# Optimization experiments

Hardware: AMD Instinct MI355X
Metric: run time of the kernel (lower is better)

Reference implementation:

```python
import jax, jax.numpy as jnp
import numpy as np
from jax import lax

B, C, H, W = 32, 512, 14, 14
NA = 9
N = H * W * NA  # 1764 anchors per image
IOU_THR = 0.3
SCORE_THR = 0.5
TOPK = 50


def setup_inputs() -> dict:
    key = jax.random.key(0)
    ks = jax.random.split(key, 8)
    def w(k, shape):
        return jax.random.normal(k, shape, jnp.float32) * 0.01  # nn.init.normal_(std=0.01)
    inp = {"features": jax.random.normal(ks[0], (B, C, H, W), jnp.float32)}
    # bbox head: 512->256 (GN32) ->128 (GN16) ->128 (GN16) -> 4*NA (1x1)
    inp["b1w"] = w(ks[1], (256, 512, 3, 3)); inp["b1b"] = jnp.zeros(256)
    inp["bg1w"] = jnp.ones(256); inp["bg1b"] = jnp.zeros(256)
    inp["b2w"] = w(ks[2], (128, 256, 3, 3)); inp["b2b"] = jnp.zeros(128)
    inp["bg2w"] = jnp.ones(128); inp["bg2b"] = jnp.zeros(128)
    inp["b3w"] = w(ks[3], (128, 128, 3, 3)); inp["b3b"] = jnp.zeros(128)
    inp["bg3w"] = jnp.ones(128); inp["bg3b"] = jnp.zeros(128)
    inp["b4w"] = w(ks[4], (4 * NA, 128, 1, 1)); inp["b4b"] = jnp.zeros(4 * NA)
    # classification head: 512->256 (GN32) ->128 (GN16) -> NA (1x1)
    inp["c1w"] = w(ks[5], (256, 512, 3, 3)); inp["c1b"] = jnp.zeros(256)
    inp["cg1w"] = jnp.ones(256); inp["cg1b"] = jnp.zeros(256)
    inp["c2w"] = w(ks[6], (128, 256, 3, 3)); inp["c2b"] = jnp.zeros(128)
    inp["cg2w"] = jnp.ones(128); inp["cg2b"] = jnp.zeros(128)
    inp["c3w"] = w(ks[7], (NA, 128, 1, 1)); inp["c3b"] = jnp.zeros(NA)
    return inp


def conv(x, w, b):
    k = w.shape[-1]
    pad = ((k // 2, k // 2), (k // 2, k // 2))
    y = lax.conv_general_dilated(x, w, (1, 1), pad, dimension_numbers=("NCHW", "OIHW", "NCHW"))
    return y + b[None, :, None, None]


def group_norm(x, w, b, groups, eps=1e-5):
    Bn, Cn, Hn, Wn = x.shape
    xg = x.reshape(Bn, groups, Cn // groups, Hn, Wn)
    mu = xg.mean(axis=(2, 3, 4), keepdims=True)
    var = xg.var(axis=(2, 3, 4), keepdims=True)
    xg = (xg - mu) * lax.rsqrt(var + eps)
    return xg.reshape(Bn, Cn, Hn, Wn) * w[None, :, None, None] + b[None, :, None, None]


def gelu(x):
    return jax.nn.gelu(x, approximate=False)  # torch nn.GELU default (erf)


def nms_single(boxes, scores):
    # boxes [N,4], scores [N]; greedy NMS, fixed-shape padded output [TOPK,5]
    valid = scores > SCORE_THR
    boxes = jnp.clip(boxes, 0.0, 1.0)
    order = jnp.argsort(-jnp.where(valid, scores, -jnp.inf))  # desc, invalid last
    b = boxes[order]; s = scores[order]; v = valid[order]
    x1 = jnp.maximum(b[:, None, 0], b[None, :, 0])
    y1 = jnp.maximum(b[:, None, 1], b[None, :, 1])
    x2 = jnp.minimum(b[:, None, 2], b[None, :, 2])
    y2 = jnp.minimum(b[:, None, 3], b[None, :, 3])
    inter = jnp.clip(x2 - x1, 0.0) * jnp.clip(y2 - y1, 0.0)
    area = (b[:, 2] - b[:, 0]) * (b[:, 3] - b[:, 1])
    iou = inter / (area[:, None] + area[None, :] - inter)
    # torch keeps when iou < thr; NaN compares False -> suppressed. Replicate exactly:
    suppress = jnp.logical_not(iou < IOU_THR)  # [N,N] bool
    idxs = jnp.arange(N)
    def body(suppressed, xs):
        row, i, vi = xs
        keep_i = vi & jnp.logical_not(suppressed[i])
        return suppressed | (keep_i & row & (idxs > i)), keep_i
    _, keep = lax.scan(body, jnp.zeros(N, bool), (suppress, idxs, v))
    kept_scores = jnp.where(keep, s, -1.0)
    topv, topi = lax.top_k(kept_scores, TOPK)  # first <=50 kept in score order
    out_boxes = jnp.where(topv[:, None] > 0.0, b[topi], 0.0)
    return jnp.concatenate([out_boxes, topv[:, None]], axis=-1)  # [TOPK, 5]; score=-1 marks pad


def _forward(features, b1w, b1b, bg1w, bg1b, b2w, b2b, bg2w, bg2b, b3w, b3b, bg3w, bg3b, b4w, b4b, c1w, c1b, cg1w, cg1b, c2w, c2b, cg2w, cg2b, c3w, c3b):
    bs = features.shape[0]
    h = group_norm(gelu(conv(features, b1w, b1b)), bg1w, bg1b, 32)
    h = group_norm(gelu(conv(h, b2w, b2b)), bg2w, bg2b, 16)
    h = group_norm(gelu(conv(h, b3w, b3b)), bg3w, bg3b, 16)
    bbox = conv(h, b4w, b4b).transpose(0, 2, 3, 1).reshape(bs, -1, 4)  # [B,N,4]
    h = group_norm(gelu(conv(features, c1w, c1b)), cg1w, cg1b, 32)
    h = group_norm(gelu(conv(h, c2w, c2b)), cg2w, cg2b, 16)
    conf = jax.nn.sigmoid(conv(h, c3w, c3b).transpose(0, 2, 3, 1).reshape(bs, -1))  # [B,N]
    return jax.vmap(nms_single)(bbox, conf)  # [B,TOPK,5]


def reference(features, b1w, b1b, bg1w, bg1b, b2w, b2b, bg2w, bg2b, b3w, b3b, bg3w, bg3b, b4w, b4b, c1w, c1b, cg1w, cg1b, c2w, c2b, cg2w, cg2b, c3w, c3b):
    return _forward(features, b1w, b1b, bg1w, bg1b, b2w, b2b, bg2w, bg2b, b3w, b3b, bg3w, bg3b, b4w, b4b, c1w, c1b, cg1w, cg1b, c2w, c2b, cg2w, cg2b, c3w, c3b)
```

## Files before the change

### kernel.cpp

```cpp
#include <hip/hip_runtime.h>
#include <hip/hip_bf16.h>
#include <math.h>

#define CHUNK 16
#define NN 1764
#define SORTN 2048

typedef float v2f __attribute__((ext_vector_type(2)));

template<int Co, int Ci>
__device__ inline void seg_pack_pk(const float* __restrict__ src, float* __restrict__ dst, int i) {
  int co = i / (Ci * 9); int rem = i - co * (Ci * 9); int ci = rem / 9; int k = rem - ci * 9;
  int p = (co >> 5) * 16 + (co & 15);
  int h = (co & 31) >> 4;
  dst[((size_t)ci * (Co >> 1) + p) * 20 + 2 * k + h] = src[i];
}
template<int Co, int CiK>
__device__ inline void seg_tr(const float* __restrict__ src, float* __restrict__ dst, int i) {
  int co = i / CiK; int cik = i - co * CiK;
  dst[cik * Co + co] = src[i];
}

__global__ void wtrans_all(
  const float* __restrict__ b1w, const float* __restrict__ c1w,
  const float* __restrict__ b2w, const float* __restrict__ c2w,
  const float* __restrict__ b3w, const float* __restrict__ b4w,
  const float* __restrict__ c3w,
  float* __restrict__ wp1b, float* __restrict__ wp1c,
  float* __restrict__ wp2b, float* __restrict__ wp2c,
  float* __restrict__ wp3b, float* __restrict__ wt4b, float* __restrict__ wt3c)
{
  int j = blockIdx.x * blockDim.x + threadIdx.x;
  if (j < 1179648) { seg_pack_pk<256, 512>(b1w, wp1b, j); return; } j -= 1179648;
  if (j < 1179648) { seg_pack_pk<256, 512>(c1w, wp1c, j); return; } j -= 1179648;
  if (j < 294912)  { seg_pack_pk<128, 256>(b2w, wp2b, j); return; } j -= 294912;
  if (j < 294912)  { seg_pack_pk<128, 256>(c2w, wp2c, j); return; } j -= 294912;
  if (j < 147456)  { seg_pack_pk<128, 128>(b3w, wp3b, j); return; } j -= 147456;
  if (j < 4608)    { seg_tr<36, 128>(b4w, wt4b, j); return; }  j -= 4608;
  if (j < 1152)    { seg_tr<9, 128>(c3w, wt3c, j); return; }
}

template<int COPT>
__global__ __launch_bounds__(256, 2) void conv3x3_part(
    const float* __restrict__ in0, const float* __restrict__ in1,
    const float* __restrict__ wt0, const float* __restrict__ wt1,
    float* __restrict__ po0, float* __restrict__ po1,
    int Cin, int Cout, int cobPerHead, int cinPerSplit, size_t sStride)
{
  constexpr int NP = COPT / 2;
  constexpr int NPP = 16 * NP;
  constexpr int NPAIR = 8 * NPP;
  const int tid = threadIdx.x;
  const int bx  = blockIdx.x;
  const int b   = blockIdx.y;
  const int s   = blockIdx.z;
  const int head = bx / cobPerHead;
  const int cob  = bx - head * cobPerHead;
  const float* in  = head ? in1  : in0;
  const float* wt  = head ? wt1  : wt0;
  float* po        = head ? po1  : po0;
  const int co0 = cob * (16 * COPT);

  const int col = tid & 15;
  const int r   = tid >> 4;
  const bool ract = r < 14;

  __shared__ float tile[2][CHUNK][16][16];
  __shared__ float wbuf[2][8][NPP][20];

  {
    float* tz = &tile[0][0][0][0];
    for (int i = tid; i < 2 * CHUNK * 256; i += 256) tz[i] = 0.0f;
  }
  __syncthreads();

  const int p = tid;
  const bool pa = p < 196;
  const int prow = p / 14, pcol = p - prow * 14;
  const float* inb = in + (size_t)b * Cin * 196;
  const int cb0 = (s * cinPerSplit) / CHUNK;
  const int nch = cinPerSplit / CHUNK;
  const int CoutH = Cout >> 1;

  const int sciL = tid / NPP;
  const int spp  = tid - sciL * NPP;
  const bool sact = tid < NPAIR;
  const int spidx = ((co0 >> 5) + (spp >> 4)) * 16 + (spp & 15);

  if (pa) {
#pragma unroll
    for (int ci = 0; ci < CHUNK; ++ci)
      tile[0][ci][prow + 1][pcol + 1] = inb[(cb0 * CHUNK + ci) * 196 + p];
  }
  if (sact) {
    const float4* src = (const float4*)(wt + ((size_t)(cb0 * CHUNK + sciL) * CoutH + spidx) * 20);
    float4 q0 = src[0], q1 = src[1], q2 = src[2], q3 = src[3], q4 = src[4];
    float4* dst = (float4*)&wbuf[0][sciL][spp][0];
    dst[0] = q0; dst[1] = q1; dst[2] = q2; dst[3] = q3; dst[4] = q4;
  }
  __syncthreads();

  v2f acc[NP][14];
#pragma unroll
  for (int g = 0; g < NP; ++g)
#pragma unroll
    for (int j = 0; j < 14; ++j) acc[g][j] = (v2f)(0.0f);

  int wcur = 0;
  for (int lcb = 0; lcb < nch; ++lcb) {
    const int cbg = cb0 + lcb;
    const int cur = lcb & 1;
    const bool more = (lcb + 1 < nch);
    float v[CHUNK];
    if (more && pa) {
#pragma unroll
      for (int ci = 0; ci < CHUNK; ++ci)
        v[ci] = inb[((cbg + 1) * CHUNK + ci) * 196 + p];
    }
#pragma unroll
    for (int half = 0; half < 2; ++half) {
      const bool hasNext = (half == 0) || more;
      const int nbase = (half == 0) ? (cbg * CHUNK + 8) : ((cbg + 1) * CHUNK);
      float4 q0, q1, q2, q3, q4;
      if (hasNext && sact) {
        const float4* src = (const float4*)(wt + ((size_t)(nbase + sciL) * CoutH + spidx) * 20);
        q0 = src[0]; q1 = src[1]; q2 = src[2]; q3 = src[3]; q4 = src[4];
      }
      if (ract) {
        __builtin_amdgcn_s_setprio(1);
#pragma unroll
        for (int ciL = 0; ciL < 8; ++ciL) {
          const int ci = half * 8 + ciL;
          v2f w2[NP][9];
#pragma unroll
          for (int g = 0; g < NP; ++g) {
            const float4* wq = (const float4*)&wbuf[wcur][ciL][g * 16 + col][0];
            float4 a0 = wq[0], a1 = wq[1], a2 = wq[2], a3 = wq[3], a4 = wq[4];
            w2[g][0] = (v2f){a0.x, a0.y}; w2[g][1] = (v2f){a0.z, a0.w};
            w2[g][2] = (v2f){a1.x, a1.y}; w2[g][3] = (v2f){a1.z, a1.w};
            w2[g][4] = (v2f){a2.x, a2.y}; w2[g][5] = (v2f){a2.z, a2.w};
            w2[g][6] = (v2f){a3.x, a3.y}; w2[g][7] = (v2f){a3.z, a3.w};
            w2[g][8] = (v2f){a4.x, a4.y};
          }
          float nb[3][16];
#pragma unroll
          for (int dr = 0; dr < 3; ++dr) {
            const float4* rp = (const float4*)(&tile[cur][ci][r + dr][0]);
            float4 a = rp[0], bq = rp[1], cq = rp[2], dq = rp[3];
            nb[dr][0]  = a.x;  nb[dr][1]  = a.y;  nb[dr][2]  = a.z;  nb[dr][3]  = a.w;
            nb[dr][4]  = bq.x; nb[dr][5]  = bq.y; nb[dr][6]  = bq.z; nb[dr][7]  = bq.w;
            nb[dr][8]  = cq.x; nb[dr][9]  = cq.y; nb[dr][10] = cq.z; nb[dr][11] = cq.w;
            nb[dr][12] = dq.x; nb[dr][13] = dq.y; nb[dr][14] = dq.z; nb[dr][15] = dq.w;
          }
#pragma unroll
          for (int ky = 0; ky < 3; ++ky)
#pragma unroll
            for (int kx = 0; kx < 3; ++kx) {
#pragma unroll
              for (int g = 0; g < NP; ++g) {
                v2f w = w2[g][ky * 3 + kx];
#pragma unroll
                for (int j = 0; j < 14; ++j) {
                  float s_ = nb[ky][j + kx];
                  v2f nbv = (v2f){s_, s_};
                  acc[g][j] = __builtin_elementwise_fma(w, nbv, acc[g][j]);
                }
              }
            }
        }
        __builtin_amdgcn_s_setprio(0);
      }
      if (hasNext && sact) {
        float4* dst = (float4*)&wbuf[wcur ^ 1][sciL][spp][0];
        dst[0] = q0; dst[1] = q1; dst[2] = q2; dst[3] = q3; dst[4] = q4;
      }
      if (half == 1 && more && pa) {
#pragma unroll
        for (int ci = 0; ci < CHUNK; ++ci)
          tile[1 - cur][ci][prow + 1][pcol + 1] = v[ci];
      }
      __syncthreads();
      wcur ^= 1;
    }
  }

  if (ract) {
#pragma unroll
    for (int g = 0; g < NP; ++g) {
      const int ocx = 32 * g + col;
      const int ocy = ocx + 16;
      float* opx = po + (size_t)s * sStride + ((size_t)b * Cout + co0 + ocx) * 196 + r * 14;
      float* opy = po + (size_t)s * sStride + ((size_t)b * Cout + co0 + ocy) * 196 + r * 14;
#pragma unroll
      for (int j = 0; j < 14; ++j) { opx[j] = acc[g][j].x; opy[j] = acc[g][j].y; }
    }
  }
}

template<int S>
__global__ __launch_bounds__(256) void combine_gn(
    const float* __restrict__ po0, const float* __restrict__ po1,
    const float* __restrict__ bs0, const float* __restrict__ bs1,
    const float* __restrict__ gw0, const float* __restrict__ gw1,
    const float* __restrict__ gb0, const float* __restrict__ gb1,
    float* __restrict__ out0, float* __restrict__ out1,
    int Cout, int cobPerHead, size_t sStride)
{
  const int tid = threadIdx.x, bx = blockIdx.x, b = blockIdx.y;
  const int head = bx / cobPerHead, cob = bx - head * cobPerHead;
  const float* po = head ? po1 : po0;
  const float* bs = head ? bs1 : bs0;
  const float* gw = head ? gw1 : gw0;
  const float* gb = head ? gb1 : gb0;
  float* out      = head ? out1 : out0;
  const int co0 = cob * 16;

  __shared__ float red[4][4];
  __shared__ float stats[4];

  const int p = tid;
  const bool pa = p < 196;
  float v[16];
  float s0 = 0.f, q0 = 0.f, s1 = 0.f, q1 = 0.f;
  if (pa) {
#pragma unroll
    for (int c = 0; c < 16; ++c) {
      const size_t base = ((size_t)b * Cout + co0 + c) * 196 + p;
      float x = bs[co0 + c];
#pragma unroll
      for (int s = 0; s < S; ++s) x += po[base + (size_t)s * sStride];
      float g = 0.5f * x * (1.0f + erff(x * 0.70710678118654752440f));
      v[c] = g;
      if (c < 8) { s0 += g; q0 += g * g; } else { s1 += g; q1 += g * g; }
    }
  }
#pragma unroll
  for (int off = 32; off > 0; off >>= 1) {
    s0 += __shfl_down(s0, off, 64); q0 += __shfl_down(q0, off, 64);
    s1 += __shfl_down(s1, off, 64); q1 += __shfl_down(q1, off, 64);
  }
  const int wave = tid >> 6, lane = tid & 63;
  if (lane == 0) { red[wave][0] = s0; red[wave][1] = q0; red[wave][2] = s1; red[wave][3] = q1; }
  __syncthreads();
  if (tid == 0) {
    float S0 = red[0][0] + red[1][0] + red[2][0] + red[3][0];
    float Q0 = red[0][1] + red[1][1] + red[2][1] + red[3][1];
    float S1 = red[0][2] + red[1][2] + red[2][2] + red[3][2];
    float Q1 = red[0][3] + red[1][3] + red[2][3] + red[3][3];
    float m0 = S0 * (1.0f / 1568.0f);
    float v0 = Q0 * (1.0f / 1568.0f) - m0 * m0;
    float m1 = S1 * (1.0f / 1568.0f);
    float v1 = Q1 * (1.0f / 1568.0f) - m1 * m1;
    stats[0] = m0; stats[1] = 1.0f / sqrtf(v0 + 1e-5f);
    stats[2] = m1; stats[3] = 1.0f / sqrtf(v1 + 1e-5f);
  }
  __syncthreads();
  if (pa) {
    float m0 = stats[0], i0 = stats[1], m1 = stats[2], i1 = stats[3];
#pragma unroll
    for (int c = 0; c < 16; ++c) {
      float m  = (c < 8) ? m0 : m1;
      float iv = (c < 8) ? i0 : i1;
      float y = (v[c] - m) * iv * gw[co0 + c] + gb[co0 + c];
      out[((size_t)b * Cout + co0 + c) * 196 + p] = y;
    }
  }
}

__global__ __launch_bounds__(512) void nms_kernel(
  const float* __restrict__ tb, const float* __restrict__ tc,
  const float* __restrict__ wtb, const float* __restrict__ wtc,
  const float* __restrict__ bb,  const float* __restrict__ bc,
  float* __restrict__ bbox, float* __restrict__ out)
{
  const int b = blockIdx.x, tid = threadIdx.x;
  __shared__ unsigned long long key[SORTN];
  __shared__ float sx1[NN], sy1[NN], sx2[NN], sy2[NN], sar[NN], ssc[NN];
  __shared__ unsigned char sup[NN];
  __shared__ int sV, sMin;

  if (tid == 0) sV = 0;
  for (int i = NN + tid; i < SORTN; i += 512) key[i] = 0ull;

  int cntv = 0;
  if (tid < 196) {
    const int p = tid;
    float ab[36], ac[9];
#pragma unroll
    for (int o = 0; o < 36; ++o) ab[o] = bb[o];
#pragma unroll
    for (int o = 0; o < 9; ++o)  ac[o] = bc[o];
    const float* pb = tb + (size_t)b * 128 * 196 + p;
    const float* pc = tc + (size_t)b * 128 * 196 + p;
    for (int ci = 0; ci < 128; ++ci) {
      float xb = pb[ci * 196];
      float xc = pc[ci * 196];
      const float* wB = wtb + ci * 36;
      const float* wC = wtc + ci * 9;
#pragma unroll
      for (int o = 0; o < 36; ++o) ab[o] = fmaf(wB[o], xb, ab[o]);
#pragma unroll
      for (int o = 0; o < 9; ++o)  ac[o] = fmaf(wC[o], xc, ac[o]);
    }
    float* bp = bbox + ((size_t)b * NN) * 4 + (size_t)p * 36;
#pragma unroll
    for (int o = 0; o < 36; ++o) bp[o] = ab[o];
#pragma unroll
    for (int a = 0; a < 9; ++a) {
      float s = 1.0f / (1.0f + expf(-ac[a]));
      const int n = p * 9 + a;
      unsigned rank = (unsigned)(NN - 1 - n);
      unsigned long long k;
      if (s > 0.5f) { k = (((unsigned long long)__float_as_uint(s)) << 32) | rank; cntv++; }
      else k = (unsigned long long)rank;
      key[n] = k;
    }
  }
  atomicAdd(&sV, cntv);
  __syncthreads();
  const int V = sV;

  for (int kk = 2; kk <= SORTN; kk <<= 1) {
    for (int j = kk >> 1; j > 0; j >>= 1) {
      for (int i = tid; i < SORTN; i += 512) {
        int ixj = i ^ j;
        if (ixj > i) {
          unsigned long long a = key[i], c = key[ixj];
          bool dirDesc = ((i & kk) == 0);
          if ((a < c) == dirDesc) { key[i] = c; key[ixj] = a; }
        }
      }
      __syncthreads();
    }
  }

  const float* bbb = bbox + (size_t)b * NN * 4;
  for (int i = tid; i < V; i += 512) {
    unsigned long long k = key[i];
    int idx = NN - 1 - (int)(unsigned)(k & 0xFFFFFFFFull);
    float s = __uint_as_float((unsigned)(k >> 32));
    const float* bp = bbb + (size_t)idx * 4;
    float x1 = fminf(fmaxf(bp[0], 0.0f), 1.0f);
    float y1 = fminf(fmaxf(bp[1], 0.0f), 1.0f);
    float x2 = fminf(fmaxf(bp[2], 0.0f), 1.0f);
    float y2 = fminf(fmaxf(bp[3], 0.0f), 1.0f);
    sx1[i] = x1; sy1[i] = y1; sx2[i] = x2; sy2[i] = y2;
    sar[i] = (x2 - x1) * (y2 - y1);
    ssc[i] = s;
    sup[i] = 0;
  }
  __syncthreads();

  int kept = 0, cur = 0;
  float* ob = out + (size_t)b * 50 * 5;
  while (kept < 50 && cur < V) {
    int nxt = -1;
    for (int base = cur; base < V; base += 512) {
      if (tid == 0) sMin = 0x7FFFFFFF;
      __syncthreads();
      int i = base + tid;
      if (i < V && !sup[i]) atomicMin(&sMin, i);
      __syncthreads();
      if (sMin != 0x7FFFFFFF) { nxt = sMin; break; }
    }
    if (nxt < 0) break;
    float kx1 = sx1[nxt], ky1 = sy1[nxt], kx2 = sx2[nxt], ky2 = sy2[nxt], ka = sar[nxt];
    if (tid == 0) {
      float* rr = ob + kept * 5;
      rr[0] = kx1; rr[1] = ky1; rr[2] = kx2; rr[3] = ky2; rr[4] = ssc[nxt];
    }
    kept++;
    for (int jj = nxt + 1 + tid; jj < V; jj += 512) {
      if (!sup[jj]) {
        float xx1 = fmaxf(kx1, sx1[jj]);
        float yy1 = fmaxf(ky1, sy1[jj]);
        float xx2 = fminf(kx2, sx2[jj]);
        float yy2 = fminf(ky2, sy2[jj]);
        float inter = fmaxf(xx2 - xx1, 0.0f) * fmaxf(yy2 - yy1, 0.0f);
        float iou = inter / ((ka + sar[jj]) - inter);
        if (!(iou < 0.3f)) sup[jj] = 1;
      }
    }
    cur = nxt + 1;
    __syncthreads();
  }
  for (int rr = kept + tid; rr < 50; rr += 512) {
    float* qq = ob + rr * 5;
    qq[0] = 0.0f; qq[1] = 0.0f; qq[2] = 0.0f; qq[3] = 0.0f; qq[4] = -1.0f;
  }
}

extern "C" void kernel_launch(void* const* d_in, const int* in_sizes, int n_in,
                              void* d_out, int out_size, void* d_ws, size_t ws_size,
                              hipStream_t stream)
{
  const float* features = (const float*)d_in[0];
  const float* b1w = (const float*)d_in[1];  const float* b1b = (const float*)d_in[2];
  const float* bg1w = (const float*)d_in[3]; const float* bg1b = (const float*)d_in[4];
  const float* b2w = (const float*)d_in[5];  const float* b2b = (const float*)d_in[6];
  const float* bg2w = (const float*)d_in[7]; const float* bg2b = (const float*)d_in[8];
  const float* b3w = (const float*)d_in[9];  const float* b3b = (const float*)d_in[10];
  const float* bg3w = (const float*)d_in[11]; const float* bg3b = (const float*)d_in[12];
  const float* b4w = (const float*)d_in[13]; const float* b4b = (const float*)d_in[14];
  const float* c1w = (const float*)d_in[15]; const float* c1b = (const float*)d_in[16];
  const float* cg1w = (const float*)d_in[17]; const float* cg1b = (const float*)d_in[18];
  const float* c2w = (const float*)d_in[19]; const float* c2b = (const float*)d_in[20];
  const float* cg2w = (const float*)d_in[21]; const float* cg2b = (const float*)d_in[22];
  const float* c3w = (const float*)d_in[23]; const float* c3b = (const float*)d_in[24];

  float* ws = (float*)d_ws;
  float* wp1b = ws; ws += 1310720;
  float* wp1c = ws; ws += 1310720;
  float* wp2b = ws; ws += 327680;
  float* wp2c = ws; ws += 327680;
  float* wp3b = ws; ws += 163840;
  float* wt4b = ws; ws += 4608;
  float* wt3c = ws; ws += 1152;
  float* t1b = ws; ws += 1605632;
  float* t1c = ws; ws += 1605632;
  float* t2b = ws; ws += 802816;
  float* t2c = ws; ws += 802816;
  float* P   = ws; ws += 12845056;
  float* bbox = ws; ws += 225792;
  float* conf = ws; ws += 56448;
  float* t3b = t1b;
  (void)conf;

  wtrans_all<<<12119, 256, 0, stream>>>(b1w, c1w, b2w, c2w, b3w, b4w, c3w,
                                        wp1b, wp1c, wp2b, wp2c, wp3b, wt4b, wt3c);

  {
    const size_t sStr = (size_t)32 * 256 * 196;
    conv3x3_part<4><<<dim3(8, 32, 2), 256, 0, stream>>>(
        features, features, wp1b, wp1c, P, P + 2 * sStr, 512, 256, 4, 256, sStr);
    combine_gn<2><<<dim3(32, 32), 256, 0, stream>>>(
        P, P + 2 * sStr, b1b, c1b, bg1w, cg1w, bg1b, cg1b, t1b, t1c, 256, 16, sStr);
  }
  {
    const size_t sStr = (size_t)32 * 128 * 196;
    conv3x3_part<4><<<dim3(4, 32, 4), 256, 0, stream>>>(
        t1b, t1c, wp2b, wp2c, P, P + 4 * sStr, 256, 128, 2, 64, sStr);
    combine_gn<4><<<dim3(16, 32), 256, 0, stream>>>(
        P, P + 4 * sStr, b2b, c2b, bg2w, cg2w, bg2b, cg2b, t2b, t2c, 128, 8, sStr);
  }
  {
    const size_t sStr = (size_t)32 * 128 * 196;
    conv3x3_part<2><<<dim3(4, 32, 4), 256, 0, stream>>>(
        t2b, t2b, wp3b, wp3b, P, P, 128, 128, 4, 32, sStr);
    combine_gn<4><<<dim3(8, 32), 256, 0, stream>>>(
        P, P, b3b, b3b, bg3w, bg3w, bg3b, bg3b, t3b, t3b, 128, 8, sStr);
  }

  nms_kernel<<<32, 512, 0, stream>>>(t3b, t2c, wt4b, wt3c, b4b, c3b, bbox, (float*)d_out);
}
```

Baseline: 743.4 us.

## Replace first-layer 3x3 convolutions with Winograd F(2x2,3x3) batched GEMM

The first 512->256 conv for both heads now runs as Winograd F(2,3): the filters are transformed into 16 tap positions, the input is transformed into 4x4 tiles, 16 per-position GEMMs over 512 channels are done in a double-buffered LDS kernel, and an output transform is fused with bias, GELU and GroupNorm. The aim is to cut the multiply count of the dominant layer by about 2.25x. In exchange it adds large intermediate V and M buffers and extra global memory traffic, and Winograd arithmetic can change fp32 rounding slightly. The s_setprio hints are also removed from the remaining direct-conv kernel.

```diff
diff --git a/kernel.cpp b/kernel.cpp
--- a/kernel.cpp
+++ b/kernel.cpp
@@ -21,23 +21,282 @@
   dst[cik * Co + co] = src[i];
 }
 
+__device__ inline void seg_wino_u(const float* __restrict__ src, float* __restrict__ dst, int i) {
+  int ci = i >> 8;
+  int co = i & 255;
+  const float* g = src + ((size_t)co * 512 + ci) * 9;
+  float g00=g[0],g01=g[1],g02=g[2],g10=g[3],g11=g[4],g12=g[5],g20=g[6],g21=g[7],g22=g[8];
+  float a[4][3];
+  a[0][0]=g00; a[0][1]=g01; a[0][2]=g02;
+  a[1][0]=0.5f*(g00+g10+g20); a[1][1]=0.5f*(g01+g11+g21); a[1][2]=0.5f*(g02+g12+g22);
+  a[2][0]=0.5f*(g00-g10+g20); a[2][1]=0.5f*(g01-g11+g21); a[2][2]=0.5f*(g02-g12+g22);
+  a[3][0]=g20; a[3][1]=g21; a[3][2]=g22;
+  const int p = (co >> 5) * 16 + (co & 15);
+  const int h = (co & 31) >> 4;
+#pragma unroll
+  for (int r4 = 0; r4 < 4; ++r4) {
+    float u0 = a[r4][0];
+    float u1 = 0.5f * (a[r4][0] + a[r4][1] + a[r4][2]);
+    float u2 = 0.5f * (a[r4][0] - a[r4][1] + a[r4][2]);
+    float u3 = a[r4][2];
+    float uv[4] = {u0, u1, u2, u3};
+#pragma unroll
+    for (int c4 = 0; c4 < 4; ++c4) {
+      int pos = r4 * 4 + c4;
+      dst[(((size_t)pos * 512 + ci) * 128 + p) * 2 + h] = uv[c4];
+    }
+  }
+}
+
 __global__ void wtrans_all(
   const float* __restrict__ b1w, const float* __restrict__ c1w,
   const float* __restrict__ b2w, const float* __restrict__ c2w,
   const float* __restrict__ b3w, const float* __restrict__ b4w,
   const float* __restrict__ c3w,
-  float* __restrict__ wp1b, float* __restrict__ wp1c,
+  float* __restrict__ ub, float* __restrict__ uc,
   float* __restrict__ wp2b, float* __restrict__ wp2c,
   float* __restrict__ wp3b, float* __restrict__ wt4b, float* __restrict__ wt3c)
 {
   int j = blockIdx.x * blockDim.x + threadIdx.x;
-  if (j < 1179648) { seg_pack_pk<256, 512>(b1w, wp1b, j); return; } j -= 1179648;
-  if (j < 1179648) { seg_pack_pk<256, 512>(c1w, wp1c, j); return; } j -= 1179648;
-  if (j < 294912)  { seg_pack_pk<128, 256>(b2w, wp2b, j); return; } j -= 294912;
-  if (j < 294912)  { seg_pack_pk<128, 256>(c2w, wp2c, j); return; } j -= 294912;
-  if (j < 147456)  { seg_pack_pk<128, 128>(b3w, wp3b, j); return; } j -= 147456;
-  if (j < 4608)    { seg_tr<36, 128>(b4w, wt4b, j); return; }  j -= 4608;
-  if (j < 1152)    { seg_tr<9, 128>(c3w, wt3c, j); return; }
+  if (j < 131072) { seg_wino_u(b1w, ub, j); return; } j -= 131072;
+  if (j < 131072) { seg_wino_u(c1w, uc, j); return; } j -= 131072;
+  if (j < 294912) { seg_pack_pk<128, 256>(b2w, wp2b, j); return; } j -= 294912;
+  if (j < 294912) { seg_pack_pk<128, 256>(c2w, wp2c, j); return; } j -= 294912;
+  if (j < 147456) { seg_pack_pk<128, 128>(b3w, wp3b, j); return; } j -= 147456;
+  if (j < 4608)   { seg_tr<36, 128>(b4w, wt4b, j); return; }  j -= 4608;
+  if (j < 1152)   { seg_tr<9, 128>(c3w, wt3c, j); return; }
+}
+
+__global__ __launch_bounds__(256) void wino_in(
+    const float* __restrict__ f, float* __restrict__ V)
+{
+  const int b = blockIdx.x, cig = blockIdx.y, tid = threadIdx.x;
+  if (tid >= 196) return;
+  const int ci = cig * 4 + tid / 49;
+  const int t  = tid % 49;
+  const int ty = t / 7, tx = t % 7;
+  const float* fp = f + ((size_t)b * 512 + ci) * 196;
+  const int y0 = 2 * ty - 1, x0 = 2 * tx - 1;
+  float d[4][4];
+#pragma unroll
+  for (int i = 0; i < 4; ++i) {
+    const int y = y0 + i;
+#pragma unroll
+    for (int j = 0; j < 4; ++j) {
+      const int x = x0 + j;
+      d[i][j] = (y >= 0 && y < 14 && x >= 0 && x < 14) ? fp[y * 14 + x] : 0.0f;
+    }
+  }
+  float tr[4][4];
+#pragma unroll
+  for (int j = 0; j < 4; ++j) {
+    tr[0][j] = d[0][j] - d[2][j];
+    tr[1][j] = d[1][j] + d[2][j];
+    tr[2][j] = d[2][j] - d[1][j];
+    tr[3][j] = d[1][j] - d[3][j];
+  }
+  const size_t m = (size_t)b * 49 + t;
+#pragma unroll
+  for (int i = 0; i < 4; ++i) {
+    float v0 = tr[i][0] - tr[i][2];
+    float v1 = tr[i][1] + tr[i][2];
+    float v2 = tr[i][2] - tr[i][1];
+    float v3 = tr[i][1] - tr[i][3];
+    V[((size_t)(i * 4 + 0) * 512 + ci) * 1568 + m] = v0;
+    V[((size_t)(i * 4 + 1) * 512 + ci) * 1568 + m] = v1;
+    V[((size_t)(i * 4 + 2) * 512 + ci) * 1568 + m] = v2;
+    V[((size_t)(i * 4 + 3) * 512 + ci) * 1568 + m] = v3;
+  }
+}
+
+__global__ __launch_bounds__(256, 2) void wino_gemm(
+    const float* __restrict__ V, const float* __restrict__ U, float* __restrict__ M)
+{
+  const int pos = blockIdx.x;
+  const int mb  = blockIdx.y;
+  const int q   = blockIdx.z;
+  const int head = q >> 1;
+  const int pb   = q & 1;
+  const int tid = threadIdx.x;
+  const int col = tid & 15;
+  const int r   = tid >> 4;
+
+  __shared__ float vbuf[2][16][128];
+  __shared__ float ubuf[2][16][128];
+
+  const float* Uh = U + (size_t)head * 2097152;
+  float* Mh = M + (size_t)head * 6422528;
+  const int m0 = mb * 128;
+
+  const int sci  = tid >> 4;
+  const int soff = (tid & 15) * 8;
+  const float* vsrc = V + ((size_t)pos * 512 + sci) * 1568 + m0 + soff;
+  const float* usrc = Uh + ((size_t)pos * 512 + sci) * 256 + pb * 128 + soff;
+
+  {
+    float4 a0 = *(const float4*)(vsrc);
+    float4 a1 = *(const float4*)(vsrc + 4);
+    float4 b0 = *(const float4*)(usrc);
+    float4 b1 = *(const float4*)(usrc + 4);
+    *(float4*)&vbuf[0][sci][soff] = a0; *(float4*)&vbuf[0][sci][soff + 4] = a1;
+    *(float4*)&ubuf[0][sci][soff] = b0; *(float4*)&ubuf[0][sci][soff + 4] = b1;
+  }
+  __syncthreads();
+
+  v2f acc[4][8];
+#pragma unroll
+  for (int g = 0; g < 4; ++g)
+#pragma unroll
+    for (int j = 0; j < 8; ++j) acc[g][j] = (v2f)(0.0f);
+
+  int cur = 0;
+  for (int cb = 0; cb < 32; ++cb) {
+    const bool more = (cb + 1 < 32);
+    float4 a0, a1, b0, b1;
+    if (more) {
+      const float* vs = vsrc + (size_t)(cb + 1) * 16 * 1568;
+      const float* us = usrc + (size_t)(cb + 1) * 16 * 256;
+      a0 = *(const float4*)vs; a1 = *(const float4*)(vs + 4);
+      b0 = *(const float4*)us; b1 = *(const float4*)(us + 4);
+    }
+#pragma unroll
+    for (int ci = 0; ci < 16; ++ci) {
+      v2f u2[4];
+#pragma unroll
+      for (int g = 0; g < 4; ++g)
+        u2[g] = *(const v2f*)&ubuf[cur][ci][(g * 16 + col) * 2];
+      const float4* vp = (const float4*)&vbuf[cur][ci][r * 8];
+      float4 v0 = vp[0], v1 = vp[1];
+      float vv[8] = {v0.x, v0.y, v0.z, v0.w, v1.x, v1.y, v1.z, v1.w};
+#pragma unroll
+      for (int j = 0; j < 8; ++j) {
+        v2f s2 = (v2f){vv[j], vv[j]};
+#pragma unroll
+        for (int g = 0; g < 4; ++g)
+          acc[g][j] = __builtin_elementwise_fma(u2[g], s2, acc[g][j]);
+      }
+    }
+    if (more) {
+      *(float4*)&vbuf[cur ^ 1][sci][soff] = a0; *(float4*)&vbuf[cur ^ 1][sci][soff + 4] = a1;
+      *(float4*)&ubuf[cur ^ 1][sci][soff] = b0; *(float4*)&ubuf[cur ^ 1][sci][soff + 4] = b1;
+    }
+    __syncthreads();
+    cur ^= 1;
+  }
+
+  const int mm = m0 + r * 8;
+  if (mm < 1568) {
+#pragma unroll
+    for (int g = 0; g < 4; ++g) {
+      const int p = pb * 64 + g * 16 + col;
+      const int cox = (p >> 4) * 32 + (p & 15);
+      float* ox = Mh + ((size_t)pos * 256 + cox) * 1568 + mm;
+      float* oy = ox + (size_t)16 * 1568;
+#pragma unroll
+      for (int j = 0; j < 8; ++j) { ox[j] = acc[g][j].x; oy[j] = acc[g][j].y; }
+    }
+  }
+}
+
+__global__ __launch_bounds__(256) void wino_out_gn(
+    const float* __restrict__ M,
+    const float* __restrict__ bsb, const float* __restrict__ bsc,
+    const float* __restrict__ gwb, const float* __restrict__ gwc,
+    const float* __restrict__ gbb, const float* __restrict__ gbc,
+    float* __restrict__ outb, float* __restrict__ outc)
+{
+  const int bx = blockIdx.x;
+  const int b  = blockIdx.y;
+  const int head = bx >> 4, cog = bx & 15;
+  const int tid = threadIdx.x;
+  const float* Mh = M + (size_t)head * 6422528;
+  const float* bs = head ? bsc : bsb;
+  const float* gw = head ? gwc : gwb;
+  const float* gb = head ? gbc : gbb;
+  float* out      = head ? outc : outb;
+  const int co0 = cog * 16;
+
+  __shared__ float red[4][4];
+  __shared__ float stats[4];
+
+  const bool pa = tid < 196;
+  const int csub = tid / 49;
+  const int t    = tid % 49;
+  const int ty = t / 7, tx = t % 7;
+  const size_t mt = (size_t)b * 49 + t;
+
+  float y4[4][4];
+  float s = 0.f, q = 0.f;
+  if (pa) {
+#pragma unroll
+    for (int cc = 0; cc < 4; ++cc) {
+      const int co = co0 + csub * 4 + cc;
+      const float* mp = Mh + (size_t)co * 1568 + mt;
+      float m16[16];
+#pragma unroll
+      for (int pos = 0; pos < 16; ++pos)
+        m16[pos] = mp[(size_t)pos * 401408];
+      float Z0[4], Z1[4];
+#pragma unroll
+      for (int j = 0; j < 4; ++j) {
+        Z0[j] = m16[0 * 4 + j] + m16[1 * 4 + j] + m16[2 * 4 + j];
+        Z1[j] = m16[1 * 4 + j] - m16[2 * 4 + j] - m16[3 * 4 + j];
+      }
+      const float bias = bs[co];
+      float yv[4];
+      yv[0] = Z0[0] + Z0[1] + Z0[2];
+      yv[1] = Z0[1] - Z0[2] - Z0[3];
+      yv[2] = Z1[0] + Z1[1] + Z1[2];
+      yv[3] = Z1[1] - Z1[2] - Z1[3];
+#pragma unroll
+      for (int k = 0; k < 4; ++k) {
+        float x = yv[k] + bias;
+        float g = 0.5f * x * (1.0f + erff(x * 0.70710678118654752440f));
+        y4[cc][k] = g;
+        s += g; q += g * g;
+      }
+    }
+  }
+  float s0 = (pa && csub < 2) ? s : 0.f, q0 = (pa && csub < 2) ? q : 0.f;
+  float s1 = (pa && csub >= 2) ? s : 0.f, q1 = (pa && csub >= 2) ? q : 0.f;
+#pragma unroll
+  for (int off = 32; off > 0; off >>= 1) {
+    s0 += __shfl_down(s0, off, 64); q0 += __shfl_down(q0, off, 64);
+    s1 += __shfl_down(s1, off, 64); q1 += __shfl_down(q1, off, 64);
+  }
+  const int wave = tid >> 6, lane = tid & 63;
+  if (lane == 0) { red[wave][0] = s0; red[wave][1] = q0; red[wave][2] = s1; red[wave][3] = q1; }
+  __syncthreads();
+  if (tid == 0) {
+    float S0 = red[0][0] + red[1][0] + red[2][0] + red[3][0];
+    float Q0 = red[0][1] + red[1][1] + red[2][1] + red[3][1];
+    float S1 = red[0][2] + red[1][2] + red[2][2] + red[3][2];
+    float Q1 = red[0][3] + red[1][3] + red[2][3] + red[3][3];
+    float m0 = S0 * (1.0f / 1568.0f);
+    float v0 = Q0 * (1.0f / 1568.0f) - m0 * m0;
+    float m1 = S1 * (1.0f / 1568.0f);
+    float v1 = Q1 * (1.0f / 1568.0f) - m1 * m1;
+    stats[0] = m0; stats[1] = 1.0f / sqrtf(v0 + 1e-5f);
+    stats[2] = m1; stats[3] = 1.0f / sqrtf(v1 + 1e-5f);
+  }
+  __syncthreads();
+  if (pa) {
+    const float mg = (csub < 2) ? stats[0] : stats[2];
+    const float iv = (csub < 2) ? stats[1] : stats[3];
+#pragma unroll
+    for (int cc = 0; cc < 4; ++cc) {
+      const int co = co0 + csub * 4 + cc;
+      const float w = gw[co], bb2 = gb[co];
+      float* op = out + ((size_t)b * 256 + co) * 196;
+#pragma unroll
+      for (int dy = 0; dy < 2; ++dy)
+#pragma unroll
+        for (int dx = 0; dx < 2; ++dx) {
+          float yv = (y4[cc][dy * 2 + dx] - mg) * iv * w + bb2;
+          op[(2 * ty + dy) * 14 + (2 * tx + dx)] = yv;
+        }
+    }
+  }
 }
 
 template<int COPT>
@@ -127,7 +386,6 @@
         q0 = src[0]; q1 = src[1]; q2 = src[2]; q3 = src[3]; q4 = src[4];
       }
       if (ract) {
-        __builtin_amdgcn_s_setprio(1);
 #pragma unroll
         for (int ciL = 0; ciL < 8; ++ciL) {
           const int ci = half * 8 + ciL;
@@ -168,7 +426,6 @@
               }
             }
         }
-        __builtin_amdgcn_s_setprio(0);
       }
       if (hasNext && sact) {
         float4* dst = (float4*)&wbuf[wcur ^ 1][sciL][spp][0];
@@ -409,33 +666,29 @@
   const float* c3w = (const float*)d_in[23]; const float* c3b = (const float*)d_in[24];
 
   float* ws = (float*)d_ws;
-  float* wp1b = ws; ws += 1310720;
-  float* wp1c = ws; ws += 1310720;
+  float* U    = ws; ws += 4194304;
   float* wp2b = ws; ws += 327680;
   float* wp2c = ws; ws += 327680;
   float* wp3b = ws; ws += 163840;
   float* wt4b = ws; ws += 4608;
   float* wt3c = ws; ws += 1152;
-  float* t1b = ws; ws += 1605632;
-  float* t1c = ws; ws += 1605632;
-  float* t2b = ws; ws += 802816;
-  float* t2c = ws; ws += 802816;
-  float* P   = ws; ws += 12845056;
+  float* t1b  = ws; ws += 1605632;
+  float* t1c  = ws; ws += 1605632;
+  float* t2b  = ws; ws += 802816;
+  float* t2c  = ws; ws += 802816;
+  float* V    = ws; ws += 12845056;
+  float* M    = ws; ws += 12845056;
   float* bbox = ws; ws += 225792;
-  float* conf = ws; ws += 56448;
-  float* t3b = t1b;
-  (void)conf;
-
-  wtrans_all<<<12119, 256, 0, stream>>>(b1w, c1w, b2w, c2w, b3w, b4w, c3w,
-                                        wp1b, wp1c, wp2b, wp2c, wp3b, wt4b, wt3c);
-
-  {
-    const size_t sStr = (size_t)32 * 256 * 196;
-    conv3x3_part<4><<<dim3(8, 32, 2), 256, 0, stream>>>(
-        features, features, wp1b, wp1c, P, P + 2 * sStr, 512, 256, 4, 256, sStr);
-    combine_gn<2><<<dim3(32, 32), 256, 0, stream>>>(
-        P, P + 2 * sStr, b1b, c1b, bg1w, cg1w, bg1b, cg1b, t1b, t1c, 256, 16, sStr);
-  }
+  float* P    = V;
+  float* t3b  = t1b;
+
+  wtrans_all<<<3927, 256, 0, stream>>>(b1w, c1w, b2w, c2w, b3w, b4w, c3w,
+                                       U, U + 2097152, wp2b, wp2c, wp3b, wt4b, wt3c);
+
+  wino_in<<<dim3(32, 128), 256, 0, stream>>>(features, V);
+  wino_gemm<<<dim3(16, 13, 4), 256, 0, stream>>>(V, U, M);
+  wino_out_gn<<<dim3(32, 32), 256, 0, stream>>>(M, b1b, c1b, bg1w, cg1w, bg1b, cg1b, t1b, t1c);
+
   {
     const size_t sStr = (size_t)32 * 128 * 196;
     conv3x3_part<4><<<dim3(4, 32, 4), 256, 0, stream>>>(
```

Measured after the change: 1.435 ms. 1.93x slower.
